# Kernel optimization log

Measured on AMD Instinct MI355X. Metric: run time of the kernel, lower is better.

Reference implementation:

```python
import jax, jax.numpy as jnp
import numpy as np

EPS = 1e-8

def _affine_combine(prev, curr):
    # compose affine maps: (a2,b2) o (a1,b1) = (a2*a1, a2*b1 + b2)
    a1, b1 = prev
    a2, b2 = curr
    return a2 * a1, a2 * b1 + b2

def parallel_scan_log(coeffs, values):
    # h_t = a_t * h_{t-1} + b_t  (inclusive scan along seq axis)
    a = jnp.clip(coeffs, EPS, 1.0 - EPS)
    _, h = jax.lax.associative_scan(_affine_combine, (a, values), axis=1)
    return h

def setup_inputs() -> dict:
    key = jax.random.key(0)
    kx, kz, kh = jax.random.split(key, 3)
    B, S, D, H = 4, 8192, 512, 512
    scale = 1.0 / np.sqrt(D)
    return {
        "x": jax.random.normal(kx, (B, S, D), dtype=jnp.float32),
        "W_z": jax.random.normal(kz, (H, D), dtype=jnp.float32) * scale,
        "b_z": jnp.zeros((H,), dtype=jnp.float32),
        "W_h": jax.random.normal(kh, (H, D), dtype=jnp.float32) * scale,
        "b_h": jnp.zeros((H,), dtype=jnp.float32),
    }

def reference(x, W_z, b_z, W_h, b_h):
    # z_t gates, h_tilde candidate; recurrence h_t = (1-z_t)*h_{t-1} + z_t*h~_t
    z = jax.nn.sigmoid(jnp.einsum("bsd,hd->bsh", x, W_z) + b_z)
    h_tilde = jnp.tanh(jnp.einsum("bsd,hd->bsh", x, W_h) + b_h)
    return parallel_scan_log(1.0 - z, z * h_tilde)
```

## Files before the change

kernel.cpp:

```cpp
#include <hip/hip_runtime.h>
#include <hip/hip_bf16.h>
#include <hip/hip_fp16.h>
#include <cstdint>
#include <cstddef>

typedef __bf16 bf16;
typedef __bf16 bf16x8 __attribute__((ext_vector_type(8)));
typedef float f32x4 __attribute__((ext_vector_type(4)));

static constexpr int NB = 4;
static constexpr int S  = 8192;
static constexpr int D  = 512;
static constexpr int H  = 512;
static constexpr int M  = NB * S;
static constexpr int CH = 64;
static constexpr int NC = S / CH;

#define BM 128
#define BN 128
#define BK 64

__device__ __forceinline__ void ld_lds16(void* lds, const void* g) {
  __builtin_amdgcn_global_load_lds(
      (const __attribute__((address_space(1))) uint32_t*)g,
      (__attribute__((address_space(3))) uint32_t*)lds, 16, 0, 0);
}

__global__ void cvt_swz_kernel(const float* __restrict__ src,
                               bf16* __restrict__ dst, int nblk) {
  int idx = blockIdx.x * blockDim.x + threadIdx.x;
  const int stride = gridDim.x * blockDim.x;
  for (; idx < nblk; idx += stride) {
    const int row = idx >> 6;
    const int blk = idx & 63;
    const float* s = src + (size_t)row * D + blk * 8;
    const float4 f0 = *(const float4*)s;
    const float4 f1 = *(const float4*)(s + 4);
    bf16x8 o;
    o[0] = (bf16)f0.x; o[1] = (bf16)f0.y; o[2] = (bf16)f0.z; o[3] = (bf16)f0.w;
    o[4] = (bf16)f1.x; o[5] = (bf16)f1.y; o[6] = (bf16)f1.z; o[7] = (bf16)f1.w;
    const int dblk = blk ^ (row & 7);
    *(bf16x8*)(dst + (size_t)row * D + dblk * 8) = o;
  }
}

__global__ __launch_bounds__(256, 2)
void gemm_gates(const bf16* __restrict__ Xb,
                const bf16* __restrict__ Wzb,
                const bf16* __restrict__ Whb,
                const float* __restrict__ bz,
                const float* __restrict__ bh,
                __half2* __restrict__ AB,
                float* __restrict__ cA,
                float* __restrict__ cB) {
  __shared__ __attribute__((aligned(16))) bf16 As[BM * BK];
  __shared__ __attribute__((aligned(16))) bf16 Zs[BN * BK];
  __shared__ __attribute__((aligned(16))) bf16 Hs[BN * BK];

  const int bid = blockIdx.x;
  const int swz = (bid & 7) * 128 + (bid >> 3);
  const int mt = swz >> 2;
  const int nt = swz & 3;
  const int m0 = mt * BM;
  const int n0 = nt * BN;
  const int tid = threadIdx.x;
  const int wave = tid >> 6;
  const int lane = tid & 63;
  const int wr = wave >> 1;
  const int wc = wave & 1;
  const int lr = lane & 15;
  const int lk = lane >> 4;
  const int xk = (lr & 7) << 3;

  f32x4 accz[4][4], acch[4][4];
  const f32x4 vzero = {0.f, 0.f, 0.f, 0.f};
#pragma unroll
  for (int i = 0; i < 4; ++i)
#pragma unroll
    for (int j = 0; j < 4; ++j) { accz[i][j] = vzero; acch[i][j] = vzero; }

  for (int ks = 0; ks < D / BK; ++ks) {
#pragma unroll
    for (int it = 0; it < 4; ++it) {
      const int fb = it * 256 + wave * 64;
      const int f  = fb + lane;
      const int row = f >> 3;
      const int kc  = f & 7;
      const size_t gk = (size_t)ks * BK + kc * 8;
      ld_lds16(&As[(size_t)fb * 8], Xb  + (size_t)(m0 + row) * D + gk);
      ld_lds16(&Zs[(size_t)fb * 8], Wzb + (size_t)(n0 + row) * D + gk);
      ld_lds16(&Hs[(size_t)fb * 8], Whb + (size_t)(n0 + row) * D + gk);
    }
    __syncthreads();
#pragma unroll
    for (int kk = 0; kk < 2; ++kk) {
      bf16x8 af[4], zf[4], hf[4];
      const int col = (kk * 32 + lk * 8) ^ xk;
#pragma unroll
      for (int m = 0; m < 4; ++m)
        af[m] = *(const bf16x8*)&As[(wr * 64 + m * 16 + lr) * BK + col];
#pragma unroll
      for (int n = 0; n < 4; ++n) {
        const int c = (wc * 64 + n * 16 + lr) * BK + col;
        zf[n] = *(const bf16x8*)&Zs[c];
        hf[n] = *(const bf16x8*)&Hs[c];
      }
#pragma unroll
      for (int m = 0; m < 4; ++m)
#pragma unroll
        for (int n = 0; n < 4; ++n) {
          accz[m][n] = __builtin_amdgcn_mfma_f32_16x16x32_bf16(af[m], zf[n], accz[m][n], 0, 0, 0);
          acch[m][n] = __builtin_amdgcn_mfma_f32_16x16x32_bf16(af[m], hf[n], acch[m][n], 0, 0, 0);
        }
    }
    __syncthreads();
  }

  const int cg = (m0 >> 6) + wr;
  float bzv[4], bhv[4], At[4], Bt[4];
#pragma unroll
  for (int n = 0; n < 4; ++n) {
    const int gn = n0 + wc * 64 + n * 16 + lr;
    bzv[n] = bz[gn];
    bhv[n] = bh[gn];
    At[n] = 1.f;
    Bt[n] = 0.f;
  }
#pragma unroll
  for (int m = 0; m < 4; ++m) {
#pragma unroll
    for (int n = 0; n < 4; ++n) {
      const int gn = n0 + wc * 64 + n * 16 + lr;
      float Aseg = 1.f, Bseg = 0.f;
#pragma unroll
      for (int j = 0; j < 4; ++j) {
        const int gm = m0 + wr * 64 + m * 16 + lk * 4 + j;
        const float vz = accz[m][n][j] + bzv[n];
        const float vh = acch[m][n][j] + bhv[n];
        const float z = 1.f / (1.f + __expf(-vz));
        const float e = __expf(-2.f * fabsf(vh));
        float th = (1.f - e) / (1.f + e);
        th = (vh < 0.f) ? -th : th;
        float a = 1.f - z;
        a = fminf(fmaxf(a, 1e-8f), 1.f - 1e-8f);
        const float bb = z * th;
        __half2 pk;
        pk.x = __float2half_rn(a);
        pk.y = __float2half_rn(bb);
        AB[(size_t)gm * H + gn] = pk;
        Aseg = a * Aseg;
        Bseg = a * Bseg + bb;
      }
      float pa = __shfl_xor(Aseg, 16);
      float pb = __shfl_xor(Bseg, 16);
      if (lane & 16) { Bseg = Aseg * pb + Bseg; Aseg = Aseg * pa; }
      else           { Bseg = pa * Bseg + pb;   Aseg = pa * Aseg; }
      pa = __shfl_xor(Aseg, 32);
      pb = __shfl_xor(Bseg, 32);
      if (lane & 32) { Bseg = Aseg * pb + Bseg; Aseg = Aseg * pa; }
      else           { Bseg = pa * Bseg + pb;   Aseg = pa * Aseg; }
      Bt[n] = Aseg * Bt[n] + Bseg;
      At[n] = Aseg * At[n];
    }
  }
  if (lk == 0) {
#pragma unroll
    for (int n = 0; n < 4; ++n) {
      const int gn = n0 + wc * 64 + n * 16 + lr;
      const size_t so = (size_t)cg * H + gn;
      cA[so] = At[n];
      cB[so] = Bt[n];
    }
  }
}

__global__ __launch_bounds__(256)
void scan_summary(const float* __restrict__ cA,
                  const float* __restrict__ cB,
                  float* __restrict__ pref) {
  const int w = blockIdx.x * 4 + (threadIdx.x >> 6);
  const int lane = threadIdx.x & 63;
  const int b = w >> 9, h = w & (H - 1);
  float hin = 0.f;
#pragma unroll
  for (int seg = 0; seg < 2; ++seg) {
    const int c = seg * 64 + lane;
    const size_t so = ((size_t)b * NC + c) * H + h;
    float A = cA[so], Bv = cB[so];
#pragma unroll
    for (int d = 1; d < 64; d <<= 1) {
      const float pa = __shfl_up(A, d);
      const float pb = __shfl_up(Bv, d);
      if (lane >= d) { Bv = A * pb + Bv; A = A * pa; }
    }
    float eA = __shfl_up(A, 1);
    float eB = __shfl_up(Bv, 1);
    if (lane == 0) { eA = 1.f; eB = 0.f; }
    pref[so] = eA * hin + eB;
    const float tA = __shfl(A, 63);
    const float tB = __shfl(Bv, 63);
    hin = tA * hin + tB;
  }
}

__global__ __launch_bounds__(512)
void scan_apply(const __half2* __restrict__ AB, float* __restrict__ out,
                const float* __restrict__ pref) {
  const int blk = blockIdx.x;
  const int b = blk / NC, c = blk % NC;
  const int h = threadIdx.x;
  const size_t base = ((size_t)b * S + (size_t)c * CH) * H + h;
  float hcur = pref[((size_t)b * NC + c) * H + h];
#pragma unroll 4
  for (int t = 0; t < CH; ++t) {
    const size_t off = base + (size_t)t * H;
    const float2 f = __half22float2(AB[off]);
    hcur = f.x * hcur + f.y;
    out[off] = hcur;
  }
}

extern "C" void kernel_launch(void* const* d_in, const int* in_sizes, int n_in,
                              void* d_out, int out_size, void* d_ws, size_t ws_size,
                              hipStream_t stream) {
  const float* x  = (const float*)d_in[0];
  const float* Wz = (const float*)d_in[1];
  const float* bz = (const float*)d_in[2];
  const float* Wh = (const float*)d_in[3];
  const float* bh = (const float*)d_in[4];
  float* out = (float*)d_out;

  char* ws = (char*)d_ws;
  __half2* AB = (__half2*)ws;
  bf16*  Xb   = (bf16*)(ws + (size_t)67108864);
  bf16*  Wzb  = (bf16*)(ws + (size_t)100663296);
  bf16*  Whb  = (bf16*)(ws + (size_t)101187584);
  float* cA   = (float*)(ws + (size_t)101711872);
  float* cB   = (float*)(ws + (size_t)102760448);
  float* pref = (float*)(ws + (size_t)103809024);

  cvt_swz_kernel<<<2048, 256, 0, stream>>>(x, Xb, M * (D / 8));
  cvt_swz_kernel<<<128, 256, 0, stream>>>(Wz, Wzb, H * (D / 8));
  cvt_swz_kernel<<<128, 256, 0, stream>>>(Wh, Whb, H * (D / 8));
  gemm_gates<<<(M / BM) * (H / BN), 256, 0, stream>>>(Xb, Wzb, Whb, bz, bh,
                                                      AB, cA, cB);
  scan_summary<<<NB * H / 4, 256, 0, stream>>>(cA, cB, pref);
  scan_apply<<<NB * NC, H, 0, stream>>>(AB, out, pref);
}
```

Measured before the change: 100.4 us.

## Fuse fp32-to-bf16 conversion of x into GEMM with register prefetch

Removes the standalone conversion pass over x. The GEMM now loads fp32 x into registers, converts it to bf16 and writes it swizzled into LDS, prefetching the next k-slice while the MFMAs run. This avoids writing and re-reading a 32MB bf16 copy of x and drops one kernel launch. The two weight conversions are also merged into a single launch. In exchange it uses more registers per thread and does the x conversion inside the GEMM, and it now reads fp32 x, which is twice the bytes, for each N tile.

```diff
diff --git a/kernel.cpp b/kernel.cpp
--- a/kernel.cpp
+++ b/kernel.cpp
@@ -26,26 +26,27 @@
       (__attribute__((address_space(3))) uint32_t*)lds, 16, 0, 0);
 }
 
-__global__ void cvt_swz_kernel(const float* __restrict__ src,
-                               bf16* __restrict__ dst, int nblk) {
+__global__ void cvt_w(const float* __restrict__ Wz, bf16* __restrict__ Wzb,
+                      const float* __restrict__ Wh, bf16* __restrict__ Whb) {
   int idx = blockIdx.x * blockDim.x + threadIdx.x;
-  const int stride = gridDim.x * blockDim.x;
-  for (; idx < nblk; idx += stride) {
-    const int row = idx >> 6;
-    const int blk = idx & 63;
-    const float* s = src + (size_t)row * D + blk * 8;
-    const float4 f0 = *(const float4*)s;
-    const float4 f1 = *(const float4*)(s + 4);
-    bf16x8 o;
-    o[0] = (bf16)f0.x; o[1] = (bf16)f0.y; o[2] = (bf16)f0.z; o[3] = (bf16)f0.w;
-    o[4] = (bf16)f1.x; o[5] = (bf16)f1.y; o[6] = (bf16)f1.z; o[7] = (bf16)f1.w;
-    const int dblk = blk ^ (row & 7);
-    *(bf16x8*)(dst + (size_t)row * D + dblk * 8) = o;
-  }
+  const int per = H * (D / 8);
+  const float* src; bf16* dst;
+  if (idx < per) { src = Wz; dst = Wzb; }
+  else           { src = Wh; dst = Whb; idx -= per; }
+  const int row = idx >> 6;
+  const int blk = idx & 63;
+  const float* s = src + (size_t)row * D + blk * 8;
+  const float4 f0 = *(const float4*)s;
+  const float4 f1 = *(const float4*)(s + 4);
+  bf16x8 o;
+  o[0] = (bf16)f0.x; o[1] = (bf16)f0.y; o[2] = (bf16)f0.z; o[3] = (bf16)f0.w;
+  o[4] = (bf16)f1.x; o[5] = (bf16)f1.y; o[6] = (bf16)f1.z; o[7] = (bf16)f1.w;
+  const int dblk = blk ^ (row & 7);
+  *(bf16x8*)(dst + (size_t)row * D + dblk * 8) = o;
 }
 
 __global__ __launch_bounds__(256, 2)
-void gemm_gates(const bf16* __restrict__ Xb,
+void gemm_gates(const float* __restrict__ Xf,
                 const bf16* __restrict__ Wzb,
                 const bf16* __restrict__ Whb,
                 const float* __restrict__ bz,
@@ -72,6 +73,9 @@
   const int lk = lane >> 4;
   const int xk = (lr & 7) << 3;
 
+  float4 xr[4][2];
+  const int sx_row = (tid * 8 + 0) >> 6;
+
   f32x4 accz[4][4], acch[4][4];
   const f32x4 vzero = {0.f, 0.f, 0.f, 0.f};
 #pragma unroll
@@ -79,7 +83,29 @@
 #pragma unroll
     for (int j = 0; j < 4; ++j) { accz[i][j] = vzero; acch[i][j] = vzero; }
 
+#pragma unroll
+  for (int it = 0; it < 4; ++it) {
+    const int idx = it * 256 + tid;
+    const int row = idx >> 3;
+    const int grp = idx & 7;
+    const float* gp = Xf + (size_t)(m0 + row) * D + grp * 8;
+    xr[it][0] = *(const float4*)gp;
+    xr[it][1] = *(const float4*)(gp + 4);
+  }
+
   for (int ks = 0; ks < D / BK; ++ks) {
+#pragma unroll
+    for (int it = 0; it < 4; ++it) {
+      const int idx = it * 256 + tid;
+      const int row = idx >> 3;
+      const int grp = idx & 7;
+      bf16x8 o;
+      o[0] = (bf16)xr[it][0].x; o[1] = (bf16)xr[it][0].y;
+      o[2] = (bf16)xr[it][0].z; o[3] = (bf16)xr[it][0].w;
+      o[4] = (bf16)xr[it][1].x; o[5] = (bf16)xr[it][1].y;
+      o[6] = (bf16)xr[it][1].z; o[7] = (bf16)xr[it][1].w;
+      *(bf16x8*)&As[row * BK + ((grp ^ (row & 7)) << 3)] = o;
+    }
 #pragma unroll
     for (int it = 0; it < 4; ++it) {
       const int fb = it * 256 + wave * 64;
@@ -87,11 +113,23 @@
       const int row = f >> 3;
       const int kc  = f & 7;
       const size_t gk = (size_t)ks * BK + kc * 8;
-      ld_lds16(&As[(size_t)fb * 8], Xb  + (size_t)(m0 + row) * D + gk);
       ld_lds16(&Zs[(size_t)fb * 8], Wzb + (size_t)(n0 + row) * D + gk);
       ld_lds16(&Hs[(size_t)fb * 8], Whb + (size_t)(n0 + row) * D + gk);
     }
     __syncthreads();
+
+    if (ks < D / BK - 1) {
+#pragma unroll
+      for (int it = 0; it < 4; ++it) {
+        const int idx = it * 256 + tid;
+        const int row = idx >> 3;
+        const int grp = idx & 7;
+        const float* gp = Xf + (size_t)(m0 + row) * D + (ks + 1) * BK + grp * 8;
+        xr[it][0] = *(const float4*)gp;
+        xr[it][1] = *(const float4*)(gp + 4);
+      }
+    }
+
 #pragma unroll
     for (int kk = 0; kk < 2; ++kk) {
       bf16x8 af[4], zf[4], hf[4];
@@ -232,17 +270,14 @@
 
   char* ws = (char*)d_ws;
   __half2* AB = (__half2*)ws;
-  bf16*  Xb   = (bf16*)(ws + (size_t)67108864);
-  bf16*  Wzb  = (bf16*)(ws + (size_t)100663296);
-  bf16*  Whb  = (bf16*)(ws + (size_t)101187584);
-  float* cA   = (float*)(ws + (size_t)101711872);
-  float* cB   = (float*)(ws + (size_t)102760448);
-  float* pref = (float*)(ws + (size_t)103809024);
-
-  cvt_swz_kernel<<<2048, 256, 0, stream>>>(x, Xb, M * (D / 8));
-  cvt_swz_kernel<<<128, 256, 0, stream>>>(Wz, Wzb, H * (D / 8));
-  cvt_swz_kernel<<<128, 256, 0, stream>>>(Wh, Whb, H * (D / 8));
-  gemm_gates<<<(M / BM) * (H / BN), 256, 0, stream>>>(Xb, Wzb, Whb, bz, bh,
+  bf16*  Wzb  = (bf16*)(ws + (size_t)67108864);
+  bf16*  Whb  = (bf16*)(ws + (size_t)67633152);
+  float* cA   = (float*)(ws + (size_t)68157440);
+  float* cB   = (float*)(ws + (size_t)69206016);
+  float* pref = (float*)(ws + (size_t)70254592);
+
+  cvt_w<<<2 * H * (D / 8) / 256, 256, 0, stream>>>(Wz, Wzb, Wh, Whb);
+  gemm_gates<<<(M / BM) * (H / BN), 256, 0, stream>>>(x, Wzb, Whb, bz, bh,
                                                       AB, cA, cB);
   scan_summary<<<NB * H / 4, 256, 0, stream>>>(cA, cB, pref);
   scan_apply<<<NB * NC, H, 0, stream>>>(AB, out, pref);
```

Result: faster. 91.58 us (-8.7%).
